# Optimization experiments

Measured on AMD Instinct MI355X. Metric: run time of the kernel, lower is better.

The kernel has to match this reference:

```python
import jax, jax.numpy as jnp
import numpy as np

IN_F, OUT_F = 1024, 4096
RANK, K_ROT, K_SCALE = 8, 8, 8
HID = 128
ROT_GATE_BIAS, SCALE_GATE_BIAS = -4.0, -2.5
RESIDUAL_SCALE, ADAPTER_SCALE = 1.0, 1.0
CTRL_DIM = 3 * IN_F  # cls_mean_var pooling


def setup_inputs() -> dict:
    key = jax.random.key(0)
    ks = jax.random.split(key, 12)
    inp = {
        "x": jax.random.normal(ks[0], (32, 512, IN_F), jnp.float32),
        "shared_weight": 0.02 * jax.random.normal(ks[1], (OUT_F, IN_F), jnp.float32),
        "bias": jnp.zeros((OUT_F,), jnp.float32),
        "left_basis": 0.02 * jax.random.normal(ks[2], (K_ROT, IN_F, RANK), jnp.float32),
        "right_basis": 0.02 * jax.random.normal(ks[3], (K_ROT, IN_F, RANK), jnp.float32),
        "scale_basis": 0.01 * jax.random.normal(ks[4], (K_SCALE, OUT_F), jnp.float32),
        "ctrl_w1": (1.0 / np.sqrt(CTRL_DIM)) * jax.random.normal(ks[5], (HID, CTRL_DIM), jnp.float32),
        "ctrl_b1": jnp.zeros((HID,), jnp.float32),
        "rot_coeff_w": (1.0 / np.sqrt(HID)) * jax.random.normal(ks[6], (K_ROT, HID), jnp.float32),
        "rot_coeff_b": jnp.zeros((K_ROT,), jnp.float32),
        "rot_gate_w": (1.0 / np.sqrt(HID)) * jax.random.normal(ks[7], (1, HID), jnp.float32),
        "rot_gate_b": jnp.zeros((1,), jnp.float32),
        "scale_coeff_w": (1.0 / np.sqrt(HID)) * jax.random.normal(ks[8], (K_SCALE, HID), jnp.float32),
        "scale_coeff_b": jnp.zeros((K_SCALE,), jnp.float32),
        "scale_gate_w": (1.0 / np.sqrt(HID)) * jax.random.normal(ks[9], (1, HID), jnp.float32),
        "scale_gate_b": jnp.zeros((1,), jnp.float32),
    }
    return inp


def reference(x, shared_weight, bias, left_basis, right_basis, scale_basis,
              ctrl_w1, ctrl_b1, rot_coeff_w, rot_coeff_b, rot_gate_w, rot_gate_b,
              scale_coeff_w, scale_coeff_b, scale_gate_w, scale_gate_b):
    # --- controller conditioning signal: cls_mean_var pooling over tokens ---
    cls = x[:, 0]                       # [B, D]
    mean = x.mean(axis=1)               # [B, D]
    var = x.var(axis=1)                 # unbiased=False -> ddof=0
    z = jnp.concatenate([cls, mean, var], axis=-1)  # [B, 3D]

    # --- controller MLP (inferred: hidden GELU + linear heads, sigmoid gates with constant bias) ---
    h = jax.nn.gelu(z @ ctrl_w1.T + ctrl_b1)                       # [B, HID]
    rot_coeff = h @ rot_coeff_w.T + rot_coeff_b                     # [B, K_ROT]
    rot_gate = jax.nn.sigmoid(h @ rot_gate_w.T + rot_gate_b + ROT_GATE_BIAS)[:, 0]    # [B]
    scale_coeff = h @ scale_coeff_w.T + scale_coeff_b               # [B, K_SCALE]
    scale_gate = jax.nn.sigmoid(h @ scale_gate_w.T + scale_gate_b + SCALE_GATE_BIAS)[:, 0]  # [B]

    # --- skew-symmetric basis: u v^T - v u^T, Frobenius-normalized per basis ---
    basis = jnp.einsum('kdr,ker->kde', left_basis, right_basis)
    basis = basis - jnp.swapaxes(basis, -2, -1)                     # [K, D, D]
    norm = jnp.maximum(jnp.sqrt(jnp.sum(basis * basis, axis=(1, 2))), 1e-6)
    basis = basis / norm[:, None, None]

    # --- per-sample skew and Cayley rotation: (I - S/2)^{-1} (I + S/2) ---
    skew = RESIDUAL_SCALE * jnp.einsum('bk,kde->bde', rot_coeff, basis)  # [B, D, D]
    eye = jnp.eye(skew.shape[-1], dtype=skew.dtype)
    half = 0.5 * skew
    transform = jnp.linalg.solve(eye[None] - half, eye[None] + half)    # [B, D, D]

    # --- gated residual rotation of tokens ---
    rotated_x = jnp.einsum('bnd,bdh->bnh', x, transform)
    mixed_x = x + ADAPTER_SCALE * rot_gate[:, None, None] * (rotated_x - x)

    # --- shared dense + learned-scale adapter ---
    preact = mixed_x @ shared_weight.T + bias                       # [B, N, OUT_F]
    scale_delta = jnp.tanh(jnp.einsum('bk,kh->bh', scale_coeff, scale_basis))
    scale = 1.0 + ADAPTER_SCALE * scale_gate[:, None, None] * scale_delta[:, None, :]
    return preact * scale
```

## Files before the change

### kernel.cpp

```cpp
#include <hip/hip_runtime.h>
#include <hip/hip_bf16.h>

typedef unsigned short u16;
typedef short short8 __attribute__((ext_vector_type(8)));
typedef float f32x4 __attribute__((ext_vector_type(4)));

#define B_    32
#define N_    512
#define INF   1024
#define OUTF  4096
#define ROWS  16384
#define HID_  128
#define CTRL  3072

__device__ __forceinline__ u16 f2bf(float f) {
    union { float fv; unsigned int u; } v; v.fv = f;
    unsigned int x = v.u;
    unsigned int r = (x + 0x7fffu + ((x >> 16) & 1u)) >> 16;
    return (u16)r;
}

__device__ __forceinline__ void gll16(const void* g, const void* l) {
    __builtin_amdgcn_global_load_lds(
        (__attribute__((address_space(1))) void*)(unsigned long long)g,
        (__attribute__((address_space(3))) void*)(unsigned int)(unsigned long long)l,
        16, 0, 0);
}

__device__ __forceinline__ float sel16(float4 a, float4 b, float4 c4, float4 d, int m) {
    float v = a.x;
    v = (m == 1) ? a.y : v;  v = (m == 2) ? a.z : v;  v = (m == 3) ? a.w : v;
    v = (m == 4) ? b.x : v;  v = (m == 5) ? b.y : v;  v = (m == 6) ? b.z : v;  v = (m == 7) ? b.w : v;
    v = (m == 8) ? c4.x : v; v = (m == 9) ? c4.y : v; v = (m == 10) ? c4.z : v; v = (m == 11) ? c4.w : v;
    v = (m == 12) ? d.x : v; v = (m == 13) ? d.y : v; v = (m == 14) ? d.z : v; v = (m == 15) ? d.w : v;
    return v;
}

__global__ __launch_bounds__(256) void k_stats(const float* __restrict__ x,
        u16* __restrict__ xb, float* __restrict__ ps, float* __restrict__ pq) {
    int b = blockIdx.y, bn = blockIdx.x, t = threadIdx.x;
    const float4* xp = (const float4*)(x + (size_t)b*(N_*INF) + (size_t)bn*64*INF);
    size_t obase = ((size_t)b*(N_*INF) + (size_t)bn*64*INF) >> 2;
    float sx=0, sy=0, sz=0, sw=0, qx=0, qy=0, qz=0, qw=0;
    for (int n = 0; n < 64; ++n) {
        float4 v = xp[n*256 + t];
        sx += v.x; sy += v.y; sz += v.z; sw += v.w;
        qx += v.x*v.x; qy += v.y*v.y; qz += v.z*v.z; qw += v.w*v.w;
        ushort4 o; o.x = f2bf(v.x); o.y = f2bf(v.y); o.z = f2bf(v.z); o.w = f2bf(v.w);
        ((ushort4*)xb)[obase + n*256 + t] = o;
    }
    int base = (b*8 + bn)*256 + t;
    float4 s4; s4.x=sx; s4.y=sy; s4.z=sz; s4.w=sw;
    float4 q4; q4.x=qx; q4.y=qy; q4.z=qz; q4.w=qw;
    ((float4*)ps)[base] = s4;
    ((float4*)pq)[base] = q4;
}

__global__ __launch_bounds__(256) void k_ctrl(const float* __restrict__ x,
    const float* __restrict__ ps, const float* __restrict__ pq,
    const float* __restrict__ w1, const float* __restrict__ b1,
    const float* __restrict__ rcw, const float* __restrict__ rcb,
    const float* __restrict__ rgw, const float* __restrict__ rgb,
    const float* __restrict__ scw, const float* __restrict__ scb,
    const float* __restrict__ sgw, const float* __restrict__ sgb,
    float* __restrict__ rc, float* __restrict__ rg,
    float* __restrict__ sc, float* __restrict__ sg)
{
    __shared__ float zs[CTRL];
    __shared__ float hs[HID_];
    int b = blockIdx.x, t = threadIdx.x;
    for (int d = t; d < 1024; d += 256) {
        float ssum = 0.f, qsum = 0.f;
        for (int j = 0; j < 8; ++j) {
            ssum += ps[(b*8 + j)*1024 + d];
            qsum += pq[(b*8 + j)*1024 + d];
        }
        float mean = ssum * (1.0f/512.0f);
        float var  = qsum * (1.0f/512.0f) - mean*mean;
        zs[d]        = x[(size_t)b*(N_*INF) + d];
        zs[1024 + d] = mean;
        zs[2048 + d] = var;
    }
    __syncthreads();
    int w = t >> 6, l = t & 63;
    const float4* zp = (const float4*)zs;
    for (int i = w; i < HID_; i += 4) {
        const float4* wr = (const float4*)(w1 + (size_t)i*CTRL);
        float acc = 0.f;
        #pragma unroll
        for (int c = 0; c < 12; ++c) {
            float4 a4 = wr[l + 64*c];
            float4 z4 = zp[l + 64*c];
            acc += a4.x*z4.x + a4.y*z4.y + a4.z*z4.z + a4.w*z4.w;
        }
        #pragma unroll
        for (int o2 = 32; o2 > 0; o2 >>= 1) acc += __shfl_down(acc, o2, 64);
        if (l == 0) {
            float u = acc + b1[i];
            hs[i] = 0.5f*u*(1.0f + tanhf(0.7978845608028654f*(u + 0.044715f*u*u*u)));
        }
    }
    __syncthreads();
    if (t < 8) {
        float a = rcb[t]; const float* wv = rcw + t*HID_;
        for (int i = 0; i < HID_; ++i) a += hs[i]*wv[i];
        rc[b*8 + t] = a;
    } else if (t < 16) {
        int j = t - 8;
        float a = scb[j]; const float* wv = scw + j*HID_;
        for (int i = 0; i < HID_; ++i) a += hs[i]*wv[i];
        sc[b*8 + j] = a;
    } else if (t == 16) {
        float a = rgb[0] - 4.0f;
        for (int i = 0; i < HID_; ++i) a += hs[i]*rgw[i];
        rg[b] = 1.0f/(1.0f + expf(-a));
    } else if (t == 17) {
        float a = sgb[0] - 2.5f;
        for (int i = 0; i < HID_; ++i) a += hs[i]*sgw[i];
        sg[b] = 1.0f/(1.0f + expf(-a));
    }
}

__global__ __launch_bounds__(64) void k_norms(const float* __restrict__ G,
        float* __restrict__ norms) {
    int k = blockIdx.x, t = threadIdx.x;
    int i = t >> 3, j = t & 7;
    float A  = G[(16*k + i)*128     + 16*k + j];
    float C  = G[(16*k + 8 + i)*128 + 16*k + 8 + j];
    float D  = G[(16*k + 8 + i)*128 + 16*k + j];
    float Dj = G[(16*k + 8 + j)*128 + 16*k + i];
    float term = A*C - D*Dj;
    #pragma unroll
    for (int o2 = 32; o2 > 0; o2 >>= 1) term += __shfl_down(term, o2, 64);
    if (t == 0) norms[k] = fmaxf(sqrtf(fmaxf(2.0f*term, 0.0f)), 1e-6f);
}

__global__ __launch_bounds__(256) void k_buildU(const float* __restrict__ L,
        const float* __restrict__ R, float* __restrict__ U, u16* __restrict__ Utb) {
    int idx = blockIdx.x*256 + threadIdx.x;
    int d = idx >> 7, col = idx & 127;
    int k = col >> 4, rr = col & 15;
    float v = (rr < 8) ? L[((size_t)k<<13) + (d<<3) + rr]
                       : R[((size_t)k<<13) + (d<<3) + (rr-8)];
    U[idx] = v;
    Utb[col*1024 + d] = f2bf(v);
}

__global__ __launch_bounds__(256) void k_gram(const float* __restrict__ U,
        float* __restrict__ G) {
    int e = blockIdx.x*256 + threadIdx.x;
    int i = e >> 7, j = e & 127;
    float a = 0.f;
    for (int d = 0; d < 1024; ++d) a += U[d*128 + i]*U[d*128 + j];
    G[e] = a;
}

__global__ __launch_bounds__(1024, 4) void k_solve(const float* __restrict__ G,
    const float* __restrict__ rc, const float* __restrict__ norms,
    const float* __restrict__ rg, u16* __restrict__ Ptb)
{
    __shared__ float smem[16384];
    float* prow = smem;
    float* pcol = smem + 256;
    int b = blockIdx.x, t = threadIdx.x;
    int r = t & 127, s = t >> 7;
    int kr = r >> 4, rr = r & 15;
    float a_r = rc[b*8 + kr] / norms[kr];
    int partner = (rr < 8) ? (kr*16 + 8 + rr) : (kr*16 + rr - 8);
    float sg0 = (rr < 8) ? -0.5f*a_r : 0.5f*a_r;
    float4 o0, o1, o2, o3;
    {
        const float4* Gp = (const float4*)(G + (size_t)partner*128 + 16*s);
        float4 g0 = Gp[0], g1 = Gp[1], g2 = Gp[2], g3 = Gp[3];
        int base = 16*s;
        o0.x = sg0*g0.x + ((r == base+0 ) ? 1.f : 0.f);
        o0.y = sg0*g0.y + ((r == base+1 ) ? 1.f : 0.f);
        o0.z = sg0*g0.z + ((r == base+2 ) ? 1.f : 0.f);
        o0.w = sg0*g0.w + ((r == base+3 ) ? 1.f : 0.f);
        o1.x = sg0*g1.x + ((r == base+4 ) ? 1.f : 0.f);
        o1.y = sg0*g1.y + ((r == base+5 ) ? 1.f : 0.f);
        o1.z = sg0*g1.z + ((r == base+6 ) ? 1.f : 0.f);
        o1.w = sg0*g1.w + ((r == base+7 ) ? 1.f : 0.f);
        o2.x = sg0*g2.x + ((r == base+8 ) ? 1.f : 0.f);
        o2.y = sg0*g2.y + ((r == base+9 ) ? 1.f : 0.f);
        o2.z = sg0*g2.z + ((r == base+10) ? 1.f : 0.f);
        o2.w = sg0*g2.w + ((r == base+11) ? 1.f : 0.f);
        o3.x = sg0*g3.x + ((r == base+12) ? 1.f : 0.f);
        o3.y = sg0*g3.y + ((r == base+13) ? 1.f : 0.f);
        o3.z = sg0*g3.z + ((r == base+14) ? 1.f : 0.f);
        o3.w = sg0*g3.w + ((r == base+15) ? 1.f : 0.f);
    }
    if (r == 0) {
        float4 v0 = o0, v1 = o1, v2 = o2, v3 = o3;
        if (s == 0) v0.x += 1.0f;
        *(float4*)(prow + 16*s +  0) = v0;
        *(float4*)(prow + 16*s +  4) = v1;
        *(float4*)(prow + 16*s +  8) = v2;
        *(float4*)(prow + 16*s + 12) = v3;
    }
    if (s == 0) pcol[r] = o0.x;
    __syncthreads();
    for (int c = 0; c < 128; ++c) {
        int buf = c & 1, nb = buf ^ 1;
        float fr = pcol[buf*128 + r];
        const float4* prp = (const float4*)(prow + buf*128 + 16*s);
        float4 p0 = prp[0], p1 = prp[1], p2 = prp[2], p3 = prp[3];
        float pv = prow[buf*128 + c] - 1.0f;
        float invp = 1.0f / pv;
        if (r == c) {
            int base = 16*s;
            o0.x = (base+0  == c) ? invp : o0.x*invp;
            o0.y = (base+1  == c) ? invp : o0.y*invp;
            o0.z = (base+2  == c) ? invp : o0.z*invp;
            o0.w = (base+3  == c) ? invp : o0.w*invp;
            o1.x = (base+4  == c) ? invp : o1.x*invp;
            o1.y = (base+5  == c) ? invp : o1.y*invp;
            o1.z = (base+6  == c) ? invp : o1.z*invp;
            o1.w = (base+7  == c) ? invp : o1.w*invp;
            o2.x = (base+8  == c) ? invp : o2.x*invp;
            o2.y = (base+9  == c) ? invp : o2.y*invp;
            o2.z = (base+10 == c) ? invp : o2.z*invp;
            o2.w = (base+11 == c) ? invp : o2.w*invp;
            o3.x = (base+12 == c) ? invp : o3.x*invp;
            o3.y = (base+13 == c) ? invp : o3.y*invp;
            o3.z = (base+14 == c) ? invp : o3.z*invp;
            o3.w = (base+15 == c) ? invp : o3.w*invp;
        } else {
            float fi = fr * invp;
            o0.x -= fi*p0.x; o0.y -= fi*p0.y; o0.z -= fi*p0.z; o0.w -= fi*p0.w;
            o1.x -= fi*p1.x; o1.y -= fi*p1.y; o1.z -= fi*p1.z; o1.w -= fi*p1.w;
            o2.x -= fi*p2.x; o2.y -= fi*p2.y; o2.z -= fi*p2.z; o2.w -= fi*p2.w;
            o3.x -= fi*p3.x; o3.y -= fi*p3.y; o3.z -= fi*p3.z; o3.w -= fi*p3.w;
        }
        int cn = c + 1;
        if (cn < 128) {
            if (r == cn) {
                float4 v0 = o0, v1 = o1, v2 = o2, v3 = o3;
                int base = 16*s;
                v0.x += (base+0  == cn) ? 1.f : 0.f;
                v0.y += (base+1  == cn) ? 1.f : 0.f;
                v0.z += (base+2  == cn) ? 1.f : 0.f;
                v0.w += (base+3  == cn) ? 1.f : 0.f;
                v1.x += (base+4  == cn) ? 1.f : 0.f;
                v1.y += (base+5  == cn) ? 1.f : 0.f;
                v1.z += (base+6  == cn) ? 1.f : 0.f;
                v1.w += (base+7  == cn) ? 1.f : 0.f;
                v2.x += (base+8  == cn) ? 1.f : 0.f;
                v2.y += (base+9  == cn) ? 1.f : 0.f;
                v2.z += (base+10 == cn) ? 1.f : 0.f;
                v2.w += (base+11 == cn) ? 1.f : 0.f;
                v3.x += (base+12 == cn) ? 1.f : 0.f;
                v3.y += (base+13 == cn) ? 1.f : 0.f;
                v3.z += (base+14 == cn) ? 1.f : 0.f;
                v3.w += (base+15 == cn) ? 1.f : 0.f;
                *(float4*)(prow + nb*128 + 16*s +  0) = v0;
                *(float4*)(prow + nb*128 + 16*s +  4) = v1;
                *(float4*)(prow + nb*128 + 16*s +  8) = v2;
                *(float4*)(prow + nb*128 + 16*s + 12) = v3;
            }
            if (s == (cn >> 4)) pcol[nb*128 + r] = sel16(o0, o1, o2, o3, cn & 15);
        }
        __syncthreads();
    }
    float as_ = rc[b*8 + s] / norms[s];
    float gg = rg[b];
    float na = -gg * as_, pa = gg * as_;
    smem[(16*s +  0)*128 + r] = na*o2.x;
    smem[(16*s +  1)*128 + r] = na*o2.y;
    smem[(16*s +  2)*128 + r] = na*o2.z;
    smem[(16*s +  3)*128 + r] = na*o2.w;
    smem[(16*s +  4)*128 + r] = na*o3.x;
    smem[(16*s +  5)*128 + r] = na*o3.y;
    smem[(16*s +  6)*128 + r] = na*o3.z;
    smem[(16*s +  7)*128 + r] = na*o3.w;
    smem[(16*s +  8)*128 + r] = pa*o0.x;
    smem[(16*s +  9)*128 + r] = pa*o0.y;
    smem[(16*s + 10)*128 + r] = pa*o0.z;
    smem[(16*s + 11)*128 + r] = pa*o0.w;
    smem[(16*s + 12)*128 + r] = pa*o1.x;
    smem[(16*s + 13)*128 + r] = pa*o1.y;
    smem[(16*s + 14)*128 + r] = pa*o1.z;
    smem[(16*s + 15)*128 + r] = pa*o1.w;
    __syncthreads();
    int r2 = t >> 3, s2 = t & 7;
    const float4* rp = (const float4*)(smem + r2*128 + 16*s2);
    float4 v0 = rp[0], v1 = rp[1], v2 = rp[2], v3 = rp[3];
    uint4 w0, w1;
    w0.x = f2bf(v0.x) | ((unsigned)f2bf(v0.y) << 16);
    w0.y = f2bf(v0.z) | ((unsigned)f2bf(v0.w) << 16);
    w0.z = f2bf(v1.x) | ((unsigned)f2bf(v1.y) << 16);
    w0.w = f2bf(v1.z) | ((unsigned)f2bf(v1.w) << 16);
    w1.x = f2bf(v2.x) | ((unsigned)f2bf(v2.y) << 16);
    w1.y = f2bf(v2.z) | ((unsigned)f2bf(v2.w) << 16);
    w1.z = f2bf(v3.x) | ((unsigned)f2bf(v3.y) << 16);
    w1.w = f2bf(v3.z) | ((unsigned)f2bf(v3.w) << 16);
    uint4* dst = (uint4*)(Ptb + ((size_t)(b*128 + r2))*128 + 16*s2);
    dst[0] = w0; dst[1] = w1;
}

__global__ __launch_bounds__(256) void k_scale(const float* __restrict__ sc,
    const float* __restrict__ sbasis, const float* __restrict__ sg,
    float* __restrict__ scl) {
    int idx = blockIdx.x*256 + threadIdx.x;
    int b = idx >> 12, o = idx & 4095;
    float a = 0.f;
    #pragma unroll
    for (int k = 0; k < 8; ++k) a += sc[b*8 + k]*sbasis[(k<<12) + o];
    scl[idx] = 1.0f + sg[b]*tanhf(a);
}

__global__ __launch_bounds__(256) void k_cvt(const float* __restrict__ in,
        u16* __restrict__ out, int n4) {
    int i = blockIdx.x*256 + threadIdx.x;
    if (i < n4) {
        float4 v = ((const float4*)in)[i];
        ushort4 o; o.x=f2bf(v.x); o.y=f2bf(v.y); o.z=f2bf(v.z); o.w=f2bf(v.w);
        ((ushort4*)out)[i] = o;
    }
}

__global__ __launch_bounds__(256) void k_gemm_bt(const u16* __restrict__ A,
    const u16* __restrict__ Bt, u16* __restrict__ C,
    int M, int N, int K, long sA_, long sB_, long sC_)
{
    A  += (size_t)blockIdx.z * sA_;
    Bt += (size_t)blockIdx.z * sB_;
    C  += (size_t)blockIdx.z * sC_;
    int bm = blockIdx.y, bn = blockIdx.x;
    __shared__ __align__(16) u16 sA[128*64];
    __shared__ __align__(16) u16 sB[128*64];
    int tid = threadIdx.x;
    int wave = tid >> 6, lane = tid & 63;
    int wbase = tid & ~63;
    int wm = wave >> 1, wn = wave & 1;
    int quad = lane >> 4, l16 = lane & 15;
    f32x4 acc[4][4];
    #pragma unroll
    for (int i = 0; i < 4; ++i)
        #pragma unroll
        for (int j = 0; j < 4; ++j) { f32x4 z4 = {0.f,0.f,0.f,0.f}; acc[i][j] = z4; }
    int nk = K >> 6;
    for (int kt = 0; kt < nk; ++kt) {
        __syncthreads();
        #pragma unroll
        for (int q2 = 0; q2 < 4; ++q2) {
            int c = q2*256 + tid, row = c >> 3, kc = c & 7;
            gll16(A  + (size_t)(bm*128 + row)*K + kt*64 + kc*8, sA + (size_t)(q2*256 + wbase)*8);
            gll16(Bt + (size_t)(bn*128 + row)*K + kt*64 + kc*8, sB + (size_t)(q2*256 + wbase)*8);
        }
        __syncthreads();
        #pragma unroll
        for (int ks = 0; ks < 2; ++ks) {
            short8 af[4], bfv[4];
            #pragma unroll
            for (int i = 0; i < 4; ++i)
                af[i] = *(const short8*)(sA + (wm*64 + i*16 + l16)*64 + ks*32 + quad*8);
            #pragma unroll
            for (int j = 0; j < 4; ++j)
                bfv[j] = *(const short8*)(sB + (wn*64 + j*16 + l16)*64 + ks*32 + quad*8);
            #pragma unroll
            for (int i = 0; i < 4; ++i)
                #pragma unroll
                for (int j = 0; j < 4; ++j)
                    acc[i][j] = __builtin_amdgcn_mfma_f32_16x16x32_bf16(af[i], bfv[j], acc[i][j], 0, 0, 0);
        }
    }
    #pragma unroll
    for (int i = 0; i < 4; ++i)
        #pragma unroll
        for (int j = 0; j < 4; ++j) {
            int gcol = bn*128 + wn*64 + j*16 + l16;
            #pragma unroll
            for (int r = 0; r < 4; ++r) {
                int grow = bm*128 + wm*64 + i*16 + quad*4 + r;
                C[(size_t)grow*N + gcol] = f2bf(acc[i][j][r]);
            }
        }
}

__global__ __launch_bounds__(512, 2) void k_main(const u16* __restrict__ xb,
    const u16* __restrict__ Wb, const u16* __restrict__ Qb,
    const u16* __restrict__ Vb, const float* __restrict__ bias,
    const float* __restrict__ scale, float* __restrict__ out)
{
    __shared__ __align__(16) u16 lds[65536];
    int flat = blockIdx.y * 16 + blockIdx.x;
    int wg   = (flat & 7) * 128 + (flat >> 3);
    int bm = wg >> 4, bn = wg & 15;
    int tid = threadIdx.x;
    int wave = tid >> 6, lane = tid & 63;
    int wm = wave >> 2, wn = wave & 3;
    int quad = lane >> 4, l16 = lane & 15;

    int srow = wave*16 + (lane >> 3);
    int scol = (((lane & 7) ^ ((lane >> 3) & 7)) << 3);
    int arow0 = bm*256 + srow;
    int brow0 = bn*256 + srow;

    int cswz0 = (quad*16)      ^ ((l16 & 7) << 4);
    int cswz1 = (64 + quad*16) ^ ((l16 & 7) << 4);
    int abase = wm*16384 + l16*128;
    int bbase = 32768 + (wn >> 1)*16384 + (wn & 1)*8192 + l16*128;

    auto stageg = [&](int kt, int bf) {
        u16* lb = lds + bf*32768;
        const u16 *As, *Bs; int str, ko;
        if (kt < 16) { As = xb; Bs = Wb; str = 1024; ko = kt*64 + scol; }
        else         { As = Qb; Bs = Vb; str = 128;  ko = (kt-16)*64 + scol; }
        #pragma unroll
        for (int i = 0; i < 2; ++i) {
            int r = i*8;
            gll16(As + (size_t)(arow0 + r)*str + ko,       lb +         wave*1024 + i*512);
            gll16(As + (size_t)(arow0 + 128 + r)*str + ko, lb +  8192 + wave*1024 + i*512);
            gll16(Bs + (size_t)(brow0 + r)*str + ko,       lb + 16384 + wave*1024 + i*512);
            gll16(Bs + (size_t)(brow0 + 128 + r)*str + ko, lb + 24576 + wave*1024 + i*512);
        }
    };

    f32x4 acc[8][4];
    #pragma unroll
    for (int m = 0; m < 8; ++m)
        #pragma unroll
        for (int n = 0; n < 4; ++n) { f32x4 z4 = {0.f,0.f,0.f,0.f}; acc[m][n] = z4; }

    stageg(0, 0);
    stageg(1, 1);
    asm volatile("s_waitcnt vmcnt(8)" ::: "memory");
    __builtin_amdgcn_s_barrier();
    __builtin_amdgcn_sched_barrier(0);

    for (int it = 0; it < 9; ++it) {
        #pragma unroll
        for (int hf = 0; hf < 2; ++hf) {
            const char* lb = (const char*)lds + hf*65536;
            short8 bfr[4][2];
            #pragma unroll
            for (int n = 0; n < 4; ++n) {
                bfr[n][0] = *(const short8*)(lb + bbase + cswz0 + n*2048);
                bfr[n][1] = *(const short8*)(lb + bbase + cswz1 + n*2048);
            }
            if (hf == 0) { if (it >= 1) stageg(2*it + 1, 1); }
            else         { if (it <= 7) stageg(2*it + 2, 0); }
            __builtin_amdgcn_s_setprio(1);
            #pragma unroll
            for (int m = 0; m < 8; ++m) {
                short8 a0 = *(const short8*)(lb + abase + cswz0 + m*2048);
                short8 a1 = *(const short8*)(lb + abase + cswz1 + m*2048);
                #pragma unroll
                for (int n = 0; n < 4; ++n) {
                    acc[m][n] = __builtin_amdgcn_mfma_f32_16x16x32_bf16(a0, bfr[n][0], acc[m][n], 0, 0, 0);
                    acc[m][n] = __builtin_amdgcn_mfma_f32_16x16x32_bf16(a1, bfr[n][1], acc[m][n], 0, 0, 0);
                }
            }
            __builtin_amdgcn_s_setprio(0);
            __builtin_amdgcn_sched_barrier(0);
            asm volatile("s_waitcnt vmcnt(0)" ::: "memory");
            __builtin_amdgcn_s_barrier();
            __builtin_amdgcn_sched_barrier(0);
        }
    }

    const float* scrow = scale + (bm >> 1)*4096;
    #pragma unroll
    for (int n = 0; n < 4; ++n) {
        int gcol = bn*256 + wn*64 + n*16 + l16;
        float bc = bias[gcol];
        float sv = scrow[gcol];
        #pragma unroll
        for (int m = 0; m < 8; ++m) {
            int growb = bm*256 + wm*128 + m*16 + quad*4;
            #pragma unroll
            for (int r = 0; r < 4; ++r)
                out[(size_t)(growb + r)*4096 + gcol] = (acc[m][n][r] + bc) * sv;
        }
    }
}

extern "C" void kernel_launch(void* const* d_in, const int* in_sizes, int n_in,
                              void* d_out, int out_size, void* d_ws, size_t ws_size,
                              hipStream_t stream)
{
    const float* x     = (const float*)d_in[0];
    const float* Wsh   = (const float*)d_in[1];
    const float* bias  = (const float*)d_in[2];
    const float* left  = (const float*)d_in[3];
    const float* right = (const float*)d_in[4];
    const float* sbasis= (const float*)d_in[5];
    const float* w1    = (const float*)d_in[6];
    const float* b1    = (const float*)d_in[7];
    const float* rcw   = (const float*)d_in[8];
    const float* rcb   = (const float*)d_in[9];
    const float* rgw   = (const float*)d_in[10];
    const float* rgb   = (const float*)d_in[11];
    const float* scw   = (const float*)d_in[12];
    const float* scb   = (const float*)d_in[13];
    const float* sgw   = (const float*)d_in[14];
    const float* sgb   = (const float*)d_in[15];
    float* out = (float*)d_out;
    (void)in_sizes; (void)n_in; (void)out_size; (void)ws_size;

    char* wsp = (char*)d_ws;
    size_t off = 0;
    auto take = [&](size_t bytes) -> char* {
        char* p = wsp + off;
        off = (off + bytes + 255) & ~(size_t)255;
        return p;
    };
    u16*   xb   = (u16*)  take((size_t)ROWS*INF*2);
    u16*   Wb   = (u16*)  take((size_t)OUTF*INF*2);
    u16*   Utb  = (u16*)  take((size_t)128*1024*2);
    u16*   Yb   = (u16*)  take((size_t)ROWS*128*2);
    u16*   Qb   = (u16*)  take((size_t)ROWS*128*2);
    u16*   Vb   = (u16*)  take((size_t)OUTF*128*2);
    u16*   Ptb  = (u16*)  take((size_t)32*128*128*2);
    float* Uf   = (float*)take((size_t)1024*128*4);
    float* Gf   = (float*)take((size_t)128*128*4);
    float* ps   = (float*)take((size_t)32*8*1024*4);
    float* pq   = (float*)take((size_t)32*8*1024*4);
    float* rc   = (float*)take(32*8*4);
    float* sc   = (float*)take(32*8*4);
    float* rg   = (float*)take(32*4);
    float* sg   = (float*)take(32*4);
    float* nrm  = (float*)take(8*4);
    float* scl  = (float*)take((size_t)32*4096*4);

    k_cvt   <<<dim3(4096),   dim3(256), 0, stream>>>(Wsh, Wb, OUTF*INF/4);
    k_stats <<<dim3(8,32),   dim3(256), 0, stream>>>(x, xb, ps, pq);
    k_buildU<<<dim3(512),    dim3(256), 0, stream>>>(left, right, Uf, Utb);
    k_gram  <<<dim3(64),     dim3(256), 0, stream>>>(Uf, Gf);
    k_norms <<<dim3(8),      dim3(64),  0, stream>>>(Gf, nrm);
    k_ctrl  <<<dim3(32),     dim3(256), 0, stream>>>(x, ps, pq, w1, b1, rcw, rcb,
                                                     rgw, rgb, scw, scb, sgw, sgb,
                                                     rc, rg, sc, sg);
    k_solve <<<dim3(32),     dim3(1024), 0, stream>>>(Gf, rc, nrm, rg, Ptb);
    k_scale <<<dim3(512),    dim3(256), 0, stream>>>(sc, sbasis, sg, scl);
    k_gemm_bt<<<dim3(1,128,1), dim3(256), 0, stream>>>(xb, Utb, Yb, ROWS, 128, 1024, 0L, 0L, 0L);
    k_gemm_bt<<<dim3(1,4,32),  dim3(256), 0, stream>>>(Yb, Ptb, Qb, 512, 128, 128,
                                                       (long)512*128, (long)128*128, (long)512*128);
    k_gemm_bt<<<dim3(1,32,1),  dim3(256), 0, stream>>>(Wb, Utb, Vb, OUTF, 128, 1024, 0L, 0L, 0L);
    k_main  <<<dim3(16,64), dim3(512), 0, stream>>>(xb, Wb, Qb, Vb, bias, scl, out);
}
```

Baseline: 784.9 us.

## Interleave GEMM main loop into four phases with finer-grained global-to-LDS prefetch

Restructures the bf16 MFMA main loop from two half-iterations per step into 18 K-tiles, each split into four phases. Each phase issues one quarter of the next tile's global-to-LDS loads, reads two A fragments from LDS and runs 16 MFMAs, separated by barriers. The intent is to spread memory traffic evenly across the compute and overlap LDS reads with MFMA issue. In exchange it adds more barriers per tile, and the prologue now waits for the first tile to fully land before starting.

```diff
diff --git a/kernel.cpp b/kernel.cpp
--- a/kernel.cpp
+++ b/kernel.cpp
@@ -402,19 +402,14 @@
     int abase = wm*16384 + l16*128;
     int bbase = 32768 + (wn >> 1)*16384 + (wn & 1)*8192 + l16*128;
 
-    auto stageg = [&](int kt, int bf) {
-        u16* lb = lds + bf*32768;
-        const u16 *As, *Bs; int str, ko;
-        if (kt < 16) { As = xb; Bs = Wb; str = 1024; ko = kt*64 + scol; }
-        else         { As = Qb; Bs = Vb; str = 128;  ko = (kt-16)*64 + scol; }
-        #pragma unroll
-        for (int i = 0; i < 2; ++i) {
-            int r = i*8;
-            gll16(As + (size_t)(arow0 + r)*str + ko,       lb +         wave*1024 + i*512);
-            gll16(As + (size_t)(arow0 + 128 + r)*str + ko, lb +  8192 + wave*1024 + i*512);
-            gll16(Bs + (size_t)(brow0 + r)*str + ko,       lb + 16384 + wave*1024 + i*512);
-            gll16(Bs + (size_t)(brow0 + 128 + r)*str + ko, lb + 24576 + wave*1024 + i*512);
-        }
+    auto stage2 = [&](int kt, int p) {
+        u16* lb = lds + (kt & 1)*32768 + p*8192;
+        const u16* S; int str, ko;
+        if (kt < 16) { S = (p < 2) ? xb : Wb; str = 1024; ko = kt*64 + scol; }
+        else         { S = (p < 2) ? Qb : Vb; str = 128;  ko = (kt-16)*64 + scol; }
+        int r0 = ((p < 2) ? arow0 : brow0) + (p & 1)*128;
+        gll16(S + (size_t)(r0    )*str + ko, lb + wave*1024);
+        gll16(S + (size_t)(r0 + 8)*str + ko, lb + wave*1024 + 512);
     };
 
     f32x4 acc[8][4];
@@ -423,38 +418,44 @@
         #pragma unroll
         for (int n = 0; n < 4; ++n) { f32x4 z4 = {0.f,0.f,0.f,0.f}; acc[m][n] = z4; }
 
-    stageg(0, 0);
-    stageg(1, 1);
-    asm volatile("s_waitcnt vmcnt(8)" ::: "memory");
+    #pragma unroll
+    for (int p = 0; p < 4; ++p) stage2(0, p);
+    asm volatile("s_waitcnt vmcnt(0)" ::: "memory");
     __builtin_amdgcn_s_barrier();
     __builtin_amdgcn_sched_barrier(0);
 
-    for (int it = 0; it < 9; ++it) {
-        #pragma unroll
-        for (int hf = 0; hf < 2; ++hf) {
-            const char* lb = (const char*)lds + hf*65536;
-            short8 bfr[4][2];
+    for (int t = 0; t < 18; ++t) {
+        const char* lb = (const char*)lds + (t & 1)*65536;
+        short8 bfr[4][2];
+        #pragma unroll
+        for (int p = 0; p < 4; ++p) {
+            if (p == 0) {
+                #pragma unroll
+                for (int n = 0; n < 4; ++n) {
+                    bfr[n][0] = *(const short8*)(lb + bbase + cswz0 + n*2048);
+                    bfr[n][1] = *(const short8*)(lb + bbase + cswz1 + n*2048);
+                }
+            }
+            short8 a0 = *(const short8*)(lb + abase + cswz0 + (2*p    )*2048);
+            short8 a1 = *(const short8*)(lb + abase + cswz1 + (2*p    )*2048);
+            short8 a2 = *(const short8*)(lb + abase + cswz0 + (2*p + 1)*2048);
+            short8 a3 = *(const short8*)(lb + abase + cswz1 + (2*p + 1)*2048);
+            if (t < 17) stage2(t + 1, p);
+            __builtin_amdgcn_s_barrier();
+            asm volatile("s_waitcnt lgkmcnt(0)" ::: "memory");
+            __builtin_amdgcn_sched_barrier(0);
+            __builtin_amdgcn_s_setprio(1);
+            int m0 = 2*p, m1 = 2*p + 1;
             #pragma unroll
             for (int n = 0; n < 4; ++n) {
-                bfr[n][0] = *(const short8*)(lb + bbase + cswz0 + n*2048);
-                bfr[n][1] = *(const short8*)(lb + bbase + cswz1 + n*2048);
-            }
-            if (hf == 0) { if (it >= 1) stageg(2*it + 1, 1); }
-            else         { if (it <= 7) stageg(2*it + 2, 0); }
-            __builtin_amdgcn_s_setprio(1);
-            #pragma unroll
-            for (int m = 0; m < 8; ++m) {
-                short8 a0 = *(const short8*)(lb + abase + cswz0 + m*2048);
-                short8 a1 = *(const short8*)(lb + abase + cswz1 + m*2048);
-                #pragma unroll
-                for (int n = 0; n < 4; ++n) {
-                    acc[m][n] = __builtin_amdgcn_mfma_f32_16x16x32_bf16(a0, bfr[n][0], acc[m][n], 0, 0, 0);
-                    acc[m][n] = __builtin_amdgcn_mfma_f32_16x16x32_bf16(a1, bfr[n][1], acc[m][n], 0, 0, 0);
-                }
+                acc[m0][n] = __builtin_amdgcn_mfma_f32_16x16x32_bf16(a0, bfr[n][0], acc[m0][n], 0, 0, 0);
+                acc[m0][n] = __builtin_amdgcn_mfma_f32_16x16x32_bf16(a1, bfr[n][1], acc[m0][n], 0, 0, 0);
+                acc[m1][n] = __builtin_amdgcn_mfma_f32_16x16x32_bf16(a2, bfr[n][0], acc[m1][n], 0, 0, 0);
+                acc[m1][n] = __builtin_amdgcn_mfma_f32_16x16x32_bf16(a3, bfr[n][1], acc[m1][n], 0, 0, 0);
             }
             __builtin_amdgcn_s_setprio(0);
             __builtin_amdgcn_sched_barrier(0);
-            asm volatile("s_waitcnt vmcnt(0)" ::: "memory");
+            if (p == 3) asm volatile("s_waitcnt vmcnt(0)" ::: "memory");
             __builtin_amdgcn_s_barrier();
             __builtin_amdgcn_sched_barrier(0);
         }
```

New measurement: 794.6 us. No clear change (+1.2%).
